# Kernel tuning notes

Hardware: AMD Instinct MI355X
Metric: run time of the kernel (lower is better)

## Reference

```python
import jax, jax.numpy as jnp
import numpy as np

N_NODES = 50000
N_EDGES = 800000
IN_F = 64
OUT_F = 64
HEADS = 4
ALPHA = 0.2  # LeakyReLU negative slope


def setup_inputs() -> dict:
    key = jax.random.key(0)
    k1, k2, k3, k4, k5, k6 = jax.random.split(key, 6)
    x = jax.random.normal(k1, (N_NODES, IN_F), dtype=jnp.float32)
    src = jax.random.randint(k2, (N_EDGES,), 0, N_NODES)
    dst = jax.random.randint(k3, (N_EDGES,), 0, N_NODES)
    edge_index = jnp.stack([src, dst]).astype(jnp.int64)
    # learned params: per-head projection + attention vectors (GAT)
    W = jax.random.normal(k4, (HEADS, IN_F, OUT_F), dtype=jnp.float32) * 0.1
    a_src = jax.random.normal(k5, (HEADS, OUT_F), dtype=jnp.float32) * 0.1
    a_dst = jax.random.normal(k6, (HEADS, OUT_F), dtype=jnp.float32) * 0.1
    return {"x": x, "edge_index": edge_index, "W": W, "a_src": a_src, "a_dst": a_dst}


def reference(x, edge_index, W, a_src, a_dst):
    N = x.shape[0]
    src, dst = edge_index[0], edge_index[1]
    # per-head projection: [N, H, O]
    h = jnp.einsum('nf,hfo->nho', x, W)
    # node-level attention halves: [N, H]
    s_src = jnp.einsum('nho,ho->nh', h, a_src)
    s_dst = jnp.einsum('nho,ho->nh', h, a_dst)
    # edge logits with LeakyReLU: [E, H]
    e = jax.nn.leaky_relu(s_src[src] + s_dst[dst], negative_slope=ALPHA)
    # segment softmax over incoming edges of each destination node
    e_max = jax.ops.segment_max(e, dst, num_segments=N)  # [N, H]
    e_exp = jnp.exp(e - e_max[dst])
    denom = jax.ops.segment_sum(e_exp, dst, num_segments=N)  # [N, H]
    attn = e_exp / (denom[dst] + 1e-16)  # [E, H]
    # weighted scatter-aggregation: [N, H, O]
    msg = h[src] * attn[:, :, None]
    out = jax.ops.segment_sum(msg, dst, num_segments=N)
    # average_head=False -> concatenate heads; no bias, no activation
    return out.reshape(N, HEADS * OUT_F)
```

## Files before the change

### kernel.cpp

```cpp
#include <hip/hip_runtime.h>

#define HEADS 4
#define OUTF 64
#define INF 64
#define CAP 48
#define NG 8
#define NSUB 64
#define LDSN 6304

typedef __attribute__((ext_vector_type(8))) short bf16x8;
typedef __attribute__((ext_vector_type(4))) float f32x4;

__device__ __forceinline__ ushort f2bf(float f) {
    const unsigned u = __float_as_uint(f);
    return (ushort)((u + 0x7fffu + ((u >> 16) & 1u)) >> 16);
}

__global__ __launch_bounds__(256) void prep_kernel(
    const float* __restrict__ W, const float* __restrict__ a_src,
    const float* __restrict__ a_dst, float* __restrict__ va_s, float* __restrict__ va_d,
    ushort* __restrict__ W_packed, const int* __restrict__ ei, int* __restrict__ flag)
{
    const int t = threadIdx.x;
    if (blockIdx.x == 8) {
        if (t == 0) {
            int all0 = 1;
            #pragma unroll
            for (int k = 1; k < 64; k += 2) all0 &= (ei[k] == 0);
            *flag = all0;
        }
        const int h = t >> 6;
        const float* Wr = W + (size_t)t * 64;
        const float* as = a_src + h * 64;
        const float* ad = a_dst + h * 64;
        float s = 0.f, d = 0.f;
        #pragma unroll
        for (int o = 0; o < 64; ++o) {
            const float wv = Wr[o];
            s = fmaf(wv, as[o], s);
            d = fmaf(wv, ad[o], d);
        }
        va_s[t] = s * 1.44269504f;
        va_d[t] = d * 1.44269504f;
        return;
    }
    const int idx  = blockIdx.x * 256 + t;
    const int tile = idx >> 7;
    const int st   = (idx >> 6) & 1;
    const int l    = idx & 63;
    const int o_g  = tile * 16 + (l & 15);
    const int hh   = o_g >> 6;
    const int oo   = o_g & 63;
    const int k0   = st * 32 + (l >> 4) * 8;
    ushort v[8];
    #pragma unroll
    for (int i = 0; i < 8; ++i)
        v[i] = f2bf(W[(size_t)hh * 4096 + (size_t)(k0 + i) * 64 + oo]);
    uint4 u;
    u.x = v[0] | ((unsigned)v[1] << 16);
    u.y = v[2] | ((unsigned)v[3] << 16);
    u.z = v[4] | ((unsigned)v[5] << 16);
    u.w = v[6] | ((unsigned)v[7] << 16);
    *reinterpret_cast<uint4*>(W_packed + (size_t)idx * 8) = u;
}

__device__ __forceinline__ void load_dst4(const int* __restrict__ ei, int i64v, int E, int e, int* dd) {
    if (i64v) {
        const int4 a = *reinterpret_cast<const int4*>(ei + 2 * (size_t)E + 2 * (size_t)e);
        const int4 b = *reinterpret_cast<const int4*>(ei + 2 * (size_t)E + 2 * (size_t)e + 4);
        dd[0] = a.x; dd[1] = a.z; dd[2] = b.x; dd[3] = b.z;
    } else {
        const int4 a = *reinterpret_cast<const int4*>(ei + (size_t)E + e);
        dd[0] = a.x; dd[1] = a.y; dd[2] = a.z; dd[3] = a.w;
    }
}
__device__ __forceinline__ void load_src4(const int* __restrict__ ei, int i64v, int E, int e, int* ss) {
    if (i64v) {
        const int4 a = *reinterpret_cast<const int4*>(ei + 2 * (size_t)e);
        const int4 b = *reinterpret_cast<const int4*>(ei + 2 * (size_t)e + 4);
        ss[0] = a.x; ss[1] = a.z; ss[2] = b.x; ss[3] = b.z;
    } else {
        const int4 a = *reinterpret_cast<const int4*>(ei + e);
        ss[0] = a.x; ss[1] = a.y; ss[2] = a.z; ss[3] = a.w;
    }
}

__global__ __launch_bounds__(1024) void fill_a(
    const float* __restrict__ x, const float* __restrict__ va_s,
    const float* __restrict__ va_d, float* __restrict__ ssrc,
    float* __restrict__ sdst, ushort* __restrict__ x_bf,
    const int* __restrict__ ei, const int* __restrict__ flag,
    int* __restrict__ gcnt, int N, int E)
{
    __shared__ int cnt[LDSN];
    const int lt = threadIdx.x;

    const int nid = blockIdx.x * 1024 + lt;
    if (nid < N) {
        const float* xr = x + (size_t)nid * 64;
        float rs[4] = {0.f, 0.f, 0.f, 0.f};
        float rd[4] = {0.f, 0.f, 0.f, 0.f};
        #pragma unroll
        for (int f4 = 0; f4 < 16; ++f4) {
            const float4 xv = *reinterpret_cast<const float4*>(xr + 4 * f4);
            uint2 xb;
            xb.x = f2bf(xv.x) | ((unsigned)f2bf(xv.y) << 16);
            xb.y = f2bf(xv.z) | ((unsigned)f2bf(xv.w) << 16);
            *reinterpret_cast<uint2*>(x_bf + (size_t)nid * 64 + 4 * f4) = xb;
            #pragma unroll
            for (int h = 0; h < 4; ++h) {
                const float4 s4 = *reinterpret_cast<const float4*>(va_s + h * 64 + 4 * f4);
                const float4 d4 = *reinterpret_cast<const float4*>(va_d + h * 64 + 4 * f4);
                rs[h] = fmaf(xv.x, s4.x, fmaf(xv.y, s4.y, fmaf(xv.z, s4.z, fmaf(xv.w, s4.w, rs[h]))));
                rd[h] = fmaf(xv.x, d4.x, fmaf(xv.y, d4.y, fmaf(xv.z, d4.z, fmaf(xv.w, d4.w, rd[h]))));
            }
        }
        *reinterpret_cast<float4*>(ssrc + (size_t)nid * 4) = make_float4(rs[0], rs[1], rs[2], rs[3]);
        *reinterpret_cast<float4*>(sdst + (size_t)nid * 4) = make_float4(rd[0], rd[1], rd[2], rd[3]);
    }

    const int g   = blockIdx.x & (NG - 1);
    const int s   = blockIdx.x >> 3;
    const int lo  = g * (N / NG);
    const int rng = (g == NG - 1) ? (N - lo) : (N / NG);
    const int chunk = ((E / NSUB) + 3) & ~3;
    const int e0  = s * chunk;
    const int e1  = min(e0 + chunk, E);
    const int i64v = *flag;

    for (int i = lt; i < rng; i += 1024) cnt[i] = 0;
    __syncthreads();

    int e = e0 + lt * 4;
    for (; e + 4 <= e1; e += 4096) {
        int dd[4];
        load_dst4(ei, i64v, E, e, dd);
        #pragma unroll
        for (int k = 0; k < 4; ++k) {
            const unsigned r = (unsigned)(dd[k] - lo);
            if (r < (unsigned)rng) atomicAdd(&cnt[r], 1);
        }
    }
    for (; e < e1; ++e) {
        const int dst = i64v ? ei[2 * (size_t)E + 2 * (size_t)e] : ei[(size_t)E + e];
        const unsigned r = (unsigned)(dst - lo);
        if (r < (unsigned)rng) atomicAdd(&cnt[r], 1);
    }
    __syncthreads();

    for (int i = lt; i < rng; i += 1024)
        gcnt[(size_t)s * N + lo + i] = cnt[i];
}

__global__ __launch_bounds__(256) void fill_b(
    int* __restrict__ gcnt, int* __restrict__ deg, int N)
{
    const int t = blockIdx.x * 256 + threadIdx.x;
    const int d = t >> 2;
    const int q = t & 3;
    if (d >= N) return;
    int v[16], ps = 0;
    #pragma unroll
    for (int j = 0; j < 16; ++j) {
        v[j] = gcnt[(size_t)(q * 16 + j) * N + d];
        ps += v[j];
    }
    int incl = ps;
    #pragma unroll
    for (int o = 1; o < 4; o <<= 1) {
        const int u = __shfl_up(incl, o, 4);
        if (q >= o) incl += u;
    }
    int run = incl - ps;
    #pragma unroll
    for (int j = 0; j < 16; ++j) {
        const int w = v[j];
        gcnt[(size_t)(q * 16 + j) * N + d] = run;
        run += w;
    }
    if (q == 3) deg[d] = incl;
}

__global__ __launch_bounds__(1024) void fill_c(
    const int* __restrict__ ei, const int* __restrict__ flag,
    const int* __restrict__ gcnt, ushort* __restrict__ csr_src, int N, int E)
{
    __shared__ int cur[LDSN];
    const int lt  = threadIdx.x;
    const int g   = blockIdx.x & (NG - 1);
    const int s   = blockIdx.x >> 3;
    const int lo  = g * (N / NG);
    const int rng = (g == NG - 1) ? (N - lo) : (N / NG);
    const int chunk = ((E / NSUB) + 3) & ~3;
    const int e0  = s * chunk;
    const int e1  = min(e0 + chunk, E);
    const int i64v = *flag;

    for (int i = lt; i < rng; i += 1024) cur[i] = gcnt[(size_t)s * N + lo + i];
    __syncthreads();

    int e = e0 + lt * 4;
    for (; e + 4 <= e1; e += 4096) {
        int dd[4];
        load_dst4(ei, i64v, E, e, dd);
        bool any = false;
        #pragma unroll
        for (int k = 0; k < 4; ++k) any |= ((unsigned)(dd[k] - lo) < (unsigned)rng);
        if (!any) continue;
        int ss[4];
        load_src4(ei, i64v, E, e, ss);
        #pragma unroll
        for (int k = 0; k < 4; ++k) {
            const unsigned r = (unsigned)(dd[k] - lo);
            if (r < (unsigned)rng) {
                const int pos = atomicAdd(&cur[r], 1);
                if (pos < CAP) csr_src[(size_t)dd[k] * CAP + pos] = (ushort)ss[k];
            }
        }
    }
    for (; e < e1; ++e) {
        const int dst = i64v ? ei[2 * (size_t)E + 2 * (size_t)e] : ei[(size_t)E + e];
        const unsigned r = (unsigned)(dst - lo);
        if (r < (unsigned)rng) {
            const int src = i64v ? ei[2 * (size_t)e] : ei[e];
            const int pos = atomicAdd(&cur[r], 1);
            if (pos < CAP) csr_src[(size_t)dst * CAP + pos] = (ushort)src;
        }
    }
}

#define ACCUM(XV, SS) do { \
    float e0 = (SS).x + sd4.x, e1 = (SS).y + sd4.y, e2 = (SS).z + sd4.z, e3 = (SS).w + sd4.w; \
    e0 = e0 >= 0.f ? e0 : 0.2f * e0; \
    e1 = e1 >= 0.f ? e1 : 0.2f * e1; \
    e2 = e2 >= 0.f ? e2 : 0.2f * e2; \
    e3 = e3 >= 0.f ? e3 : 0.2f * e3; \
    const float w0 = exp2f(e0), w1 = exp2f(e1), w2 = exp2f(e2), w3 = exp2f(e3); \
    const float f0 = __uint_as_float((XV).x << 16); \
    const float f1 = __uint_as_float((XV).x & 0xffff0000u); \
    const float f2 = __uint_as_float((XV).y << 16); \
    const float f3 = __uint_as_float((XV).y & 0xffff0000u); \
    A00 = fmaf(w0, f0, A00); A01 = fmaf(w0, f1, A01); A02 = fmaf(w0, f2, A02); A03 = fmaf(w0, f3, A03); \
    A10 = fmaf(w1, f0, A10); A11 = fmaf(w1, f1, A11); A12 = fmaf(w1, f2, A12); A13 = fmaf(w1, f3, A13); \
    A20 = fmaf(w2, f0, A20); A21 = fmaf(w2, f1, A21); A22 = fmaf(w2, f2, A22); A23 = fmaf(w2, f3, A23); \
    A30 = fmaf(w3, f0, A30); A31 = fmaf(w3, f1, A31); A32 = fmaf(w3, f2, A32); A33 = fmaf(w3, f3, A33); \
    ws0 += w0; ws1 += w1; ws2 += w2; ws3 += w3; \
} while (0)

#define CHUNK(SV, CNT) do { \
    int j = 0; \
    for (; j + 2 <= (CNT); j += 2) { \
        const int sA = __shfl((SV), g0 + j); \
        const int sB = __shfl((SV), g0 + j + 1); \
        const uint2 xA = *reinterpret_cast<const uint2*>(x_bf + ((size_t)sA << 6) + (l4 << 2)); \
        const uint2 xB = *reinterpret_cast<const uint2*>(x_bf + ((size_t)sB << 6) + (l4 << 2)); \
        const float4 pA = *reinterpret_cast<const float4*>(ssrc + 4 * (size_t)sA); \
        const float4 pB = *reinterpret_cast<const float4*>(ssrc + 4 * (size_t)sB); \
        ACCUM(xA, pA); \
        ACCUM(xB, pB); \
    } \
    if (j < (CNT)) { \
        const int sA = __shfl((SV), g0 + j); \
        const uint2 xA = *reinterpret_cast<const uint2*>(x_bf + ((size_t)sA << 6) + (l4 << 2)); \
        const float4 pA = *reinterpret_cast<const float4*>(ssrc + 4 * (size_t)sA); \
        ACCUM(xA, pA); \
    } \
} while (0)

__global__ __launch_bounds__(256) void gather_out(
    const int* __restrict__ deg, const ushort* __restrict__ csr_src,
    const ushort* __restrict__ x_bf, const float* __restrict__ ssrc,
    const float* __restrict__ sdst, const ushort* __restrict__ W_packed,
    float* __restrict__ out, int N)
{
    __shared__ ushort agg_lds[16][264];

    const int tid  = threadIdx.x;
    const int lane = tid & 63;
    const int l4   = lane & 15;
    const int g0   = lane & 48;
    const int wv   = tid >> 6;
    const int nl   = wv * 4 + (lane >> 4);
    const int n    = blockIdx.x * 16 + nl;
    const size_t base = (size_t)n * CAP;
    const int d    = min(deg[n], CAP);

    const int sv0 = (int)csr_src[base + l4];
    const int sv1 = (int)csr_src[base + 16 + l4];
    const int sv2 = (int)csr_src[base + 32 + l4];

    const float4 sd4 = *reinterpret_cast<const float4*>(sdst + (size_t)n * 4);

    float A00 = 0.f, A01 = 0.f, A02 = 0.f, A03 = 0.f;
    float A10 = 0.f, A11 = 0.f, A12 = 0.f, A13 = 0.f;
    float A20 = 0.f, A21 = 0.f, A22 = 0.f, A23 = 0.f;
    float A30 = 0.f, A31 = 0.f, A32 = 0.f, A33 = 0.f;
    float ws0 = 0.f, ws1 = 0.f, ws2 = 0.f, ws3 = 0.f;

    const int c0 = min(d, 16);
    const int c1 = min(max(d - 16, 0), 16);
    const int c2 = min(max(d - 32, 0), 16);
    CHUNK(sv0, c0);
    CHUNK(sv1, c1);
    CHUNK(sv2, c2);

    ushort* ap = &agg_lds[nl][l4 << 2];
    const float i0 = 1.f / (ws0 + 1e-16f);
    const float i1 = 1.f / (ws1 + 1e-16f);
    const float i2 = 1.f / (ws2 + 1e-16f);
    const float i3 = 1.f / (ws3 + 1e-16f);
    uint2 o;
    o.x = f2bf(A00 * i0) | ((unsigned)f2bf(A01 * i0) << 16);
    o.y = f2bf(A02 * i0) | ((unsigned)f2bf(A03 * i0) << 16);
    *reinterpret_cast<uint2*>(ap) = o;
    o.x = f2bf(A10 * i1) | ((unsigned)f2bf(A11 * i1) << 16);
    o.y = f2bf(A12 * i1) | ((unsigned)f2bf(A13 * i1) << 16);
    *reinterpret_cast<uint2*>(ap + 64) = o;
    o.x = f2bf(A20 * i2) | ((unsigned)f2bf(A21 * i2) << 16);
    o.y = f2bf(A22 * i2) | ((unsigned)f2bf(A23 * i2) << 16);
    *reinterpret_cast<uint2*>(ap + 128) = o;
    o.x = f2bf(A30 * i3) | ((unsigned)f2bf(A31 * i3) << 16);
    o.y = f2bf(A32 * i3) | ((unsigned)f2bf(A33 * i3) << 16);
    *reinterpret_cast<uint2*>(ap + 192) = o;

    __syncthreads();

    const int r    = lane & 15;
    const int kb   = (lane >> 4) * 8;
    const int hoff = wv * 64;
    const bf16x8 a0 = *reinterpret_cast<const bf16x8*>(&agg_lds[r][hoff + kb]);
    const bf16x8 a1 = *reinterpret_cast<const bf16x8*>(&agg_lds[r][hoff + 32 + kb]);

    const int drow = (lane >> 4) * 4;
    const int nb0  = blockIdx.x * 16;
    #pragma unroll
    for (int tt = 0; tt < 4; ++tt) {
        const int tile = wv * 4 + tt;
        const bf16x8 b0 = *reinterpret_cast<const bf16x8*>(W_packed + ((size_t)(tile * 2 + 0) * 64 + lane) * 8);
        const bf16x8 b1 = *reinterpret_cast<const bf16x8*>(W_packed + ((size_t)(tile * 2 + 1) * 64 + lane) * 8);
        f32x4 acc = {0.f, 0.f, 0.f, 0.f};
        acc = __builtin_amdgcn_mfma_f32_16x16x32_bf16(a0, b0, acc, 0, 0, 0);
        acc = __builtin_amdgcn_mfma_f32_16x16x32_bf16(a1, b1, acc, 0, 0, 0);
        const int col = tile * 16 + r;
        #pragma unroll
        for (int i = 0; i < 4; ++i)
            out[(size_t)(nb0 + drow + i) * 256 + col] = acc[i];
    }
}

extern "C" void kernel_launch(void* const* d_in, const int* in_sizes, int n_in,
                              void* d_out, int out_size, void* d_ws, size_t ws_size,
                              hipStream_t stream) {
    const float* x     = (const float*)d_in[0];
    const int*   ei    = (const int*)d_in[1];
    const float* W     = (const float*)d_in[2];
    const float* a_src = (const float*)d_in[3];
    const float* a_dst = (const float*)d_in[4];
    float*       out   = (float*)d_out;

    const int N = in_sizes[0] / INF;
    const int E = in_sizes[1] / 2;

    ushort* x_bf     = (ushort*)d_ws;
    ushort* W_packed = x_bf + (size_t)N * 64;
    float* ssrc      = (float*)(W_packed + 16384);
    float* sdst      = ssrc + (size_t)N * 4;
    float* va_s      = sdst + (size_t)N * 4;
    float* va_d      = va_s + 256;
    int*   deg       = (int*)(va_d + 256);
    int*   gcnt      = deg + N;
    ushort* csr_src  = (ushort*)(gcnt + (size_t)NSUB * N);
    int*   flag      = (int*)(csr_src + (size_t)N * CAP);

    prep_kernel<<<9, 256, 0, stream>>>(W, a_src, a_dst, va_s, va_d, W_packed, ei, flag);
    fill_a<<<NSUB * NG, 1024, 0, stream>>>(x, va_s, va_d, ssrc, sdst, x_bf, ei, flag, gcnt, N, E);
    fill_b<<<(N * 4 + 255) / 256, 256, 0, stream>>>(gcnt, deg, N);
    fill_c<<<NSUB * NG, 1024, 0, stream>>>(ei, flag, gcnt, csr_src, N, E);
    gather_out<<<N / 16, 256, 0, stream>>>(deg, csr_src, x_bf, ssrc, sdst, W_packed, out, N);
}
```

Measured before the change: 98.73 us.

## Precompute per-edge attention weights during CSR fill and store as bf16

Edge attention weights (leaky-relu plus exp2 of the src and dst scores) are now computed once in fill_c while the CSR is being built, and stored as packed bf16 per slot in a new csr_w array. gather_out reads these weights directly instead of gathering the ssrc float4 for each neighbour and recomputing the exponentials, so the gather loses its random ssrc reads and its exp work. In exchange, fill_c does extra random ssrc reads plus scattered 8-byte writes, the weights lose precision by being stored in bf16, and the workspace grows by N*CAP*8 bytes.

```diff
diff --git a/kernel.cpp b/kernel.cpp
--- a/kernel.cpp
+++ b/kernel.cpp
@@ -183,7 +183,9 @@
 
 __global__ __launch_bounds__(1024) void fill_c(
     const int* __restrict__ ei, const int* __restrict__ flag,
-    const int* __restrict__ gcnt, ushort* __restrict__ csr_src, int N, int E)
+    const int* __restrict__ gcnt, const float* __restrict__ ssrc,
+    const float* __restrict__ sdst, ushort* __restrict__ csr_src,
+    ushort* __restrict__ csr_w, int N, int E)
 {
     __shared__ int cur[LDSN];
     const int lt  = threadIdx.x;
@@ -214,7 +216,21 @@
             const unsigned r = (unsigned)(dd[k] - lo);
             if (r < (unsigned)rng) {
                 const int pos = atomicAdd(&cur[r], 1);
-                if (pos < CAP) csr_src[(size_t)dd[k] * CAP + pos] = (ushort)ss[k];
+                if (pos < CAP) {
+                    const size_t slot = (size_t)dd[k] * CAP + pos;
+                    csr_src[slot] = (ushort)ss[k];
+                    const float4 s4 = *reinterpret_cast<const float4*>(ssrc + 4 * (size_t)ss[k]);
+                    const float4 d4 = *reinterpret_cast<const float4*>(sdst + 4 * (size_t)dd[k]);
+                    float w0 = s4.x + d4.x, w1 = s4.y + d4.y, w2 = s4.z + d4.z, w3 = s4.w + d4.w;
+                    w0 = w0 >= 0.f ? w0 : 0.2f * w0;
+                    w1 = w1 >= 0.f ? w1 : 0.2f * w1;
+                    w2 = w2 >= 0.f ? w2 : 0.2f * w2;
+                    w3 = w3 >= 0.f ? w3 : 0.2f * w3;
+                    uint2 wp;
+                    wp.x = f2bf(exp2f(w0)) | ((unsigned)f2bf(exp2f(w1)) << 16);
+                    wp.y = f2bf(exp2f(w2)) | ((unsigned)f2bf(exp2f(w3)) << 16);
+                    *reinterpret_cast<uint2*>(csr_w + slot * 4) = wp;
+                }
             }
         }
     }
@@ -224,18 +240,30 @@
         if (r < (unsigned)rng) {
             const int src = i64v ? ei[2 * (size_t)e] : ei[e];
             const int pos = atomicAdd(&cur[r], 1);
-            if (pos < CAP) csr_src[(size_t)dst * CAP + pos] = (ushort)src;
-        }
-    }
-}
-
-#define ACCUM(XV, SS) do { \
-    float e0 = (SS).x + sd4.x, e1 = (SS).y + sd4.y, e2 = (SS).z + sd4.z, e3 = (SS).w + sd4.w; \
-    e0 = e0 >= 0.f ? e0 : 0.2f * e0; \
-    e1 = e1 >= 0.f ? e1 : 0.2f * e1; \
-    e2 = e2 >= 0.f ? e2 : 0.2f * e2; \
-    e3 = e3 >= 0.f ? e3 : 0.2f * e3; \
-    const float w0 = exp2f(e0), w1 = exp2f(e1), w2 = exp2f(e2), w3 = exp2f(e3); \
+            if (pos < CAP) {
+                const size_t slot = (size_t)dst * CAP + pos;
+                csr_src[slot] = (ushort)src;
+                const float4 s4 = *reinterpret_cast<const float4*>(ssrc + 4 * (size_t)src);
+                const float4 d4 = *reinterpret_cast<const float4*>(sdst + 4 * (size_t)dst);
+                float w0 = s4.x + d4.x, w1 = s4.y + d4.y, w2 = s4.z + d4.z, w3 = s4.w + d4.w;
+                w0 = w0 >= 0.f ? w0 : 0.2f * w0;
+                w1 = w1 >= 0.f ? w1 : 0.2f * w1;
+                w2 = w2 >= 0.f ? w2 : 0.2f * w2;
+                w3 = w3 >= 0.f ? w3 : 0.2f * w3;
+                uint2 wp;
+                wp.x = f2bf(exp2f(w0)) | ((unsigned)f2bf(exp2f(w1)) << 16);
+                wp.y = f2bf(exp2f(w2)) | ((unsigned)f2bf(exp2f(w3)) << 16);
+                *reinterpret_cast<uint2*>(csr_w + slot * 4) = wp;
+            }
+        }
+    }
+}
+
+#define ACCW(XV, WV) do { \
+    const float w0 = __uint_as_float((WV).x << 16); \
+    const float w1 = __uint_as_float((WV).x & 0xffff0000u); \
+    const float w2 = __uint_as_float((WV).y << 16); \
+    const float w3 = __uint_as_float((WV).y & 0xffff0000u); \
     const float f0 = __uint_as_float((XV).x << 16); \
     const float f1 = __uint_as_float((XV).x & 0xffff0000u); \
     const float f2 = __uint_as_float((XV).y << 16); \
@@ -247,31 +275,30 @@
     ws0 += w0; ws1 += w1; ws2 += w2; ws3 += w3; \
 } while (0)
 
-#define CHUNK(SV, CNT) do { \
+#define CHUNKW(SV, OFF, CNT) do { \
     int j = 0; \
     for (; j + 2 <= (CNT); j += 2) { \
         const int sA = __shfl((SV), g0 + j); \
         const int sB = __shfl((SV), g0 + j + 1); \
         const uint2 xA = *reinterpret_cast<const uint2*>(x_bf + ((size_t)sA << 6) + (l4 << 2)); \
         const uint2 xB = *reinterpret_cast<const uint2*>(x_bf + ((size_t)sB << 6) + (l4 << 2)); \
-        const float4 pA = *reinterpret_cast<const float4*>(ssrc + 4 * (size_t)sA); \
-        const float4 pB = *reinterpret_cast<const float4*>(ssrc + 4 * (size_t)sB); \
-        ACCUM(xA, pA); \
-        ACCUM(xB, pB); \
+        const uint2 wA = *reinterpret_cast<const uint2*>(csr_w + (base + (OFF) + j) * 4); \
+        const uint2 wB = *reinterpret_cast<const uint2*>(csr_w + (base + (OFF) + j + 1) * 4); \
+        ACCW(xA, wA); \
+        ACCW(xB, wB); \
     } \
     if (j < (CNT)) { \
         const int sA = __shfl((SV), g0 + j); \
         const uint2 xA = *reinterpret_cast<const uint2*>(x_bf + ((size_t)sA << 6) + (l4 << 2)); \
-        const float4 pA = *reinterpret_cast<const float4*>(ssrc + 4 * (size_t)sA); \
-        ACCUM(xA, pA); \
+        const uint2 wA = *reinterpret_cast<const uint2*>(csr_w + (base + (OFF) + j) * 4); \
+        ACCW(xA, wA); \
     } \
 } while (0)
 
 __global__ __launch_bounds__(256) void gather_out(
     const int* __restrict__ deg, const ushort* __restrict__ csr_src,
-    const ushort* __restrict__ x_bf, const float* __restrict__ ssrc,
-    const float* __restrict__ sdst, const ushort* __restrict__ W_packed,
-    float* __restrict__ out, int N)
+    const ushort* __restrict__ csr_w, const ushort* __restrict__ x_bf,
+    const ushort* __restrict__ W_packed, float* __restrict__ out, int N)
 {
     __shared__ ushort agg_lds[16][264];
 
@@ -289,8 +316,6 @@
     const int sv1 = (int)csr_src[base + 16 + l4];
     const int sv2 = (int)csr_src[base + 32 + l4];
 
-    const float4 sd4 = *reinterpret_cast<const float4*>(sdst + (size_t)n * 4);
-
     float A00 = 0.f, A01 = 0.f, A02 = 0.f, A03 = 0.f;
     float A10 = 0.f, A11 = 0.f, A12 = 0.f, A13 = 0.f;
     float A20 = 0.f, A21 = 0.f, A22 = 0.f, A23 = 0.f;
@@ -300,9 +325,9 @@
     const int c0 = min(d, 16);
     const int c1 = min(max(d - 16, 0), 16);
     const int c2 = min(max(d - 32, 0), 16);
-    CHUNK(sv0, c0);
-    CHUNK(sv1, c1);
-    CHUNK(sv2, c2);
+    CHUNKW(sv0, 0, c0);
+    CHUNKW(sv1, 16, c1);
+    CHUNKW(sv2, 32, c2);
 
     ushort* ap = &agg_lds[nl][l4 << 2];
     const float i0 = 1.f / (ws0 + 1e-16f);
@@ -370,11 +395,12 @@
     int*   deg       = (int*)(va_d + 256);
     int*   gcnt      = deg + N;
     ushort* csr_src  = (ushort*)(gcnt + (size_t)NSUB * N);
-    int*   flag      = (int*)(csr_src + (size_t)N * CAP);
+    ushort* csr_w    = csr_src + (size_t)N * CAP;
+    int*   flag      = (int*)(csr_w + (size_t)N * CAP * 4);
 
     prep_kernel<<<9, 256, 0, stream>>>(W, a_src, a_dst, va_s, va_d, W_packed, ei, flag);
     fill_a<<<NSUB * NG, 1024, 0, stream>>>(x, va_s, va_d, ssrc, sdst, x_bf, ei, flag, gcnt, N, E);
     fill_b<<<(N * 4 + 255) / 256, 256, 0, stream>>>(gcnt, deg, N);
-    fill_c<<<NSUB * NG, 1024, 0, stream>>>(ei, flag, gcnt, csr_src, N, E);
-    gather_out<<<N / 16, 256, 0, stream>>>(deg, csr_src, x_bf, ssrc, sdst, W_packed, out, N);
-}
+    fill_c<<<NSUB * NG, 1024, 0, stream>>>(ei, flag, gcnt, ssrc, sdst, csr_src, csr_w, N, E);
+    gather_out<<<N / 16, 256, 0, stream>>>(deg, csr_src, csr_w, x_bf, W_packed, out, N);
+}
```

New measurement: 101.9 us. 1.03x slower.
